# Performance work log

Measured on AMD Instinct MI355X. Metric: run time of the kernel, lower is better.

The kernel has to match this reference:

```python
import jax, jax.numpy as jnp
import numpy as np

B, T, D = 4, 4096, 1024
H = 16
DK = D // H
EPS = 1e-6


def _phi(x):
    return jax.nn.elu(x) + 1.0


def setup_inputs() -> dict:
    key = jax.random.key(0)
    ks = jax.random.split(key, 9)
    s = 1.0 / np.sqrt(D)
    return {
        "x": jax.random.normal(ks[0], (B, T, D), dtype=jnp.float32),
        "Wq": jax.random.uniform(ks[1], (D, D), jnp.float32, -s, s),
        "bq": jax.random.uniform(ks[2], (D,), jnp.float32, -s, s),
        "Wk": jax.random.uniform(ks[3], (D, D), jnp.float32, -s, s),
        "bk": jax.random.uniform(ks[4], (D,), jnp.float32, -s, s),
        "Wv": jax.random.uniform(ks[5], (D, D), jnp.float32, -s, s),
        "bv": jax.random.uniform(ks[6], (D,), jnp.float32, -s, s),
        "Wo": jax.random.uniform(ks[7], (D, D), jnp.float32, -s, s),
        "bo": jax.random.uniform(ks[8], (D,), jnp.float32, -s, s),
    }


def reference(x, Wq, bq, Wk, bk, Wv, bv, Wo, bo):
    Bq, Tq, _ = x.shape

    def heads(y):  # [B,T,D] -> [B,H,T,DK]
        return y.reshape(Bq, Tq, H, DK).transpose(0, 2, 1, 3)

    q = _phi(heads(x @ Wq.T + bq))
    k = _phi(heads(x @ Wk.T + bk))
    v = heads(x @ Wv.T + bv)

    # associative KV summary: [B,H,DK,DK]
    kv = jnp.einsum("bhtd,bhtm->bhdm", k, v)
    # normalizer: q . (sum_t k + eps), then +eps, reciprocal
    z = 1.0 / (jnp.einsum("bhtd,bhd->bht", q, k.sum(axis=2) + EPS) + EPS)
    out = jnp.einsum("bhtd,bhdm,bht->bhtm", q, kv, z)

    out = out.transpose(0, 2, 1, 3).reshape(Bq, Tq, -1)  # [B,T,D]
    return out @ Wo.T + bo
```

## Files before the change

### kernel.cpp

```cpp
#include <hip/hip_runtime.h>
#include <cstdint>
#include <cstddef>

typedef unsigned short u16;
typedef __bf16 bf16x8 __attribute__((ext_vector_type(8)));
typedef float  f32x4  __attribute__((ext_vector_type(4)));
typedef u16    u16x8v __attribute__((ext_vector_type(8)));
typedef u16    u16x4  __attribute__((ext_vector_type(4)));

#define EPS 1e-6f

__device__ __forceinline__ u16 f2bf(float f) {
  union { float f; unsigned int u; } v; v.f = f;
  unsigned int u = v.u + 0x7FFFu + ((v.u >> 16) & 1u);
  return (u16)(u >> 16);
}
__device__ __forceinline__ float bf2f(u16 h) {
  union { unsigned int u; float f; } v; v.u = ((unsigned int)h) << 16;
  return v.f;
}
__device__ __forceinline__ void async16(const void* g, void* l) {
  __builtin_amdgcn_global_load_lds(
      (const __attribute__((address_space(1))) void*)g,
      (__attribute__((address_space(3))) void*)l, 16, 0, 0);
}

__global__ __launch_bounds__(256) void cvt_all_kernel(
    const float* __restrict__ x,
    const float* __restrict__ w0, const float* __restrict__ w1,
    const float* __restrict__ w2, const float* __restrict__ w3,
    u16* __restrict__ xb, u16* __restrict__ o0, u16* __restrict__ o1,
    u16* __restrict__ o2, u16* __restrict__ o3) {
  const int gb = blockIdx.x;
  const float* in;
  u16* out;
  int i;
  if (gb < 8192) {
    in = x; out = xb; i = gb * 256 + threadIdx.x;
  } else {
    const int wb = gb - 8192;
    in  = (wb < 512) ? w0 : (wb < 1024) ? w1 : (wb < 1536) ? w2 : w3;
    out = (wb < 512) ? o0 : (wb < 1024) ? o1 : (wb < 1536) ? o2 : o3;
    i = (wb & 511) * 256 + threadIdx.x;
  }
  const float4* p = (const float4*)in;
  float4 a = p[2 * (size_t)i], b = p[2 * (size_t)i + 1];
  u16x8v o;
  o[0] = f2bf(a.x); o[1] = f2bf(a.y); o[2] = f2bf(a.z); o[3] = f2bf(a.w);
  o[4] = f2bf(b.x); o[5] = f2bf(b.y); o[6] = f2bf(b.z); o[7] = f2bf(b.w);
  *(u16x8v*)(out + 8 * (size_t)i) = o;
}

template <int MODE>
__global__ __launch_bounds__(512) void gemm4r(
    const u16* __restrict__ A, const u16* __restrict__ Bw,
    const float* __restrict__ bias0, const float* __restrict__ bias1,
    const float* __restrict__ bias2,
    u16* __restrict__ O0, u16* __restrict__ O1, u16* __restrict__ O2,
    float* __restrict__ Of, int K) {
  __shared__ u16 sA[2][256 * 64];
  __shared__ u16 sB[2][256 * 64];

  const int tid = threadIdx.x, wave = tid >> 6, lane = tid & 63;
  const int bm = blockIdx.x * 256, bn = blockIdx.y * 256;
  const int wmh = (wave >> 2) * 64;
  const int wq  = (wave & 3) * 32;
  const int l15 = lane & 15, l4 = lane >> 4, l7 = lane & 7;

  f32x4 acc[8][4] = {};

  const int trow = tid >> 3;
  const int sch8 = ((tid & 7) ^ (trow & 7)) * 8;

#define STG_A(buf, qm, s, kt)                                                 \
  async16(A + (size_t)(bm + (s)*128 + (qm)*64 + trow) * K + (kt) + sch8,      \
          &sA[buf][(((qm)*128 + (s)*64) + wave * 8) * 64])
#define STG_B(buf, qn, s, kt)                                                 \
  async16(Bw + (size_t)(bn + ((s)*2 + (trow >> 5)) * 64 + (qn)*32 +           \
                        (trow & 31)) * K + (kt) + sch8,                       \
          &sB[buf][(((qn)*128 + (s)*64) + wave * 8) * 64])

  bf16x8 af[4][2], bq[4][2];

#define RD_A(buf, qm)                                                         \
  _Pragma("unroll") for (int m = 0; m < 4; m++)                               \
    _Pragma("unroll") for (int kk = 0; kk < 2; kk++)                          \
      af[m][kk] = *(const bf16x8*)&sA[buf][((qm)*128 + wmh + m * 16 + l15) * 64 \
                                           + ((kk * 4 + l4) ^ l7) * 8];
#define RD_B(buf)                                                             \
  _Pragma("unroll") for (int nf = 0; nf < 4; nf++)                            \
    _Pragma("unroll") for (int kk = 0; kk < 2; kk++)                          \
      bq[nf][kk] = *(const bf16x8*)&sB[buf][((nf >> 1) * 128 + wq +           \
                                            (nf & 1) * 16 + l15) * 64 +       \
                                           ((kk * 4 + l4) ^ l7) * 8];

#define WAITV_(n) asm volatile("s_waitcnt vmcnt(" #n ")" ::: "memory")
#define WAITV(n) WAITV_(n)

#define PH_EXEC_(qm, W)                                                       \
  _Pragma("unroll") for (int kk = 0; kk < 2; kk++)                            \
    _Pragma("unroll") for (int m = 0; m < 4; m++)                             \
      _Pragma("unroll") for (int nf = 0; nf < 4; nf++)                        \
        acc[(qm)*4 + m][nf] = __builtin_amdgcn_mfma_f32_16x16x32_bf16(        \
            af[m][kk], bq[nf][kk], acc[(qm)*4 + m][nf], 0, 0, 0);             \
  asm volatile("s_waitcnt vmcnt(" #W ") lgkmcnt(0)" ::: "memory");            \
  __builtin_amdgcn_s_barrier();                                               \
  asm volatile("" ::: "memory");
#define PH_EXEC(qm, W) PH_EXEC_(qm, W)

#define ITER_BODY(kO, kE2, kO2, hasT2, hasT3, W0, W1, W2, W3)                 \
                  \
  RD_B(0); RD_A(0, 0);                                                        \
  STG_A(1, 1, 0, kO); STG_A(1, 1, 1, kO);                                     \
  PH_EXEC(0, W0);                                                             \
                                      \
  RD_A(0, 1);                                                                 \
  if (hasT2) {                                                                \
    STG_B(0, 0, 0, kE2); STG_B(0, 0, 1, kE2);                                 \
    STG_B(0, 1, 0, kE2); STG_B(0, 1, 1, kE2);                                 \
    STG_A(0, 0, 0, kE2); STG_A(0, 0, 1, kE2);                                 \
  }                                                                           \
  PH_EXEC(1, W1);                                                             \
                             \
  RD_B(1); RD_A(1, 0);                                                        \
  if (hasT2) { STG_A(0, 1, 0, kE2); STG_A(0, 1, 1, kE2); }                    \
  PH_EXEC(0, W2);                                                             \
                                      \
  RD_A(1, 1);                                                                 \
  if (hasT3) {                                                                \
    STG_B(1, 0, 0, kO2); STG_B(1, 0, 1, kO2);                                 \
    STG_B(1, 1, 0, kO2); STG_B(1, 1, 1, kO2);                                 \
    STG_A(1, 0, 0, kO2); STG_A(1, 0, 1, kO2);                                 \
  }                                                                           \
  PH_EXEC(1, W3);

  STG_B(0, 0, 0, 0);  STG_B(0, 0, 1, 0);  STG_B(0, 1, 0, 0);  STG_B(0, 1, 1, 0);
  STG_A(0, 0, 0, 0);  STG_A(0, 0, 1, 0);
  STG_A(0, 1, 0, 0);  STG_A(0, 1, 1, 0);
  STG_B(1, 0, 0, 64); STG_B(1, 0, 1, 64); STG_B(1, 1, 0, 64); STG_B(1, 1, 1, 64);
  STG_A(1, 0, 0, 64); STG_A(1, 0, 1, 64);
  WAITV(6);
  __builtin_amdgcn_s_barrier();
  asm volatile("" ::: "memory");

  const int NT = K >> 6;
  const int NI = NT >> 1;
  for (int i = 0; i < NI - 1; ++i) {
    const int kO  = (2 * i + 1) * 64;
    const int kE2 = (2 * i + 2) * 64;
    const int kO2 = (2 * i + 3) * 64;
    ITER_BODY(kO, kE2, kO2, true, true, 8, 8, 8, 8);
  }
  {
    const int kO = (NT - 1) * 64;
    ITER_BODY(kO, 0, 0, false, false, 8, 2, 0, 0);
  }
#undef STG_A
#undef STG_B
#undef RD_A
#undef RD_B
#undef WAITV
#undef WAITV_
#undef PH_EXEC
#undef PH_EXEC_
#undef ITER_BODY

  const int wm = wmh * 2;
  const int wn = (wave & 3) * 64;
  const int r0 = l4 * 4, cc = l15;
  if constexpr (MODE == 1) {
    const int mat = blockIdx.y >> 2;
    u16* outp = (mat == 0) ? O0 : (mat == 1) ? O1 : O2;
    const float* bias = (mat == 0) ? bias0 : (mat == 1) ? bias1 : bias2;
    const int act = (mat < 2);
    const int colb = (blockIdx.y & 3) * 256;
    float bvv[4];
#pragma unroll
    for (int ni = 0; ni < 4; ni++) bvv[ni] = bias[colb + wn + ni * 16 + cc];
#pragma unroll
    for (int mi = 0; mi < 8; mi++) {
#pragma unroll
      for (int j = 0; j < 4; j++) {
        const int row = bm + wm + mi * 16 + r0 + j;
#pragma unroll
        for (int ni = 0; ni < 4; ni++) {
          const int col = colb + wn + ni * 16 + cc;
          float val = acc[mi][ni][j] + bvv[ni];
          if (act) val = (val > 0.f) ? (val + 1.f) : __expf(val);
          outp[(size_t)row * 1024 + col] = f2bf(val);
        }
      }
    }
  } else {
    float bvv[4];
#pragma unroll
    for (int ni = 0; ni < 4; ni++) bvv[ni] = bias0[bn + wn + ni * 16 + cc];
#pragma unroll
    for (int mi = 0; mi < 8; mi++) {
#pragma unroll
      for (int j = 0; j < 4; j++) {
        const int row = bm + wm + mi * 16 + r0 + j;
#pragma unroll
        for (int ni = 0; ni < 4; ni++) {
          const int col = bn + wn + ni * 16 + cc;
          Of[(size_t)row * 1024 + col] = acc[mi][ni][j] + bvv[ni];
        }
      }
    }
  }
}

__global__ __launch_bounds__(256) void kv_mfma_kernel(
    const u16* __restrict__ Kb, const u16* __restrict__ Vb,
    float* __restrict__ kv_part, float* __restrict__ ksum_part) {
  const int bh = blockIdx.y;
  const int chunk = blockIdx.x;
  const int b = bh >> 4, h = bh & 15;
  const int tid = threadIdx.x, wave = tid >> 6, lane = tid & 63;

  __shared__ u16 sKT[64 * 64];
  __shared__ u16 sVT[64 * 64];

  f32x4 acc[4] = {};
  f32x4 accs[4] = {};

  union { u16x8v u; bf16x8 b; } uo;
#pragma unroll
  for (int e = 0; e < 8; e++) uo.u[e] = 0x3F80;
  const bf16x8 ones = uo.b;

  const int half = tid >> 7;
  const int j    = tid & 127;
  const int tg   = j >> 3;
  const int dg   = j & 7;
  const u16* src = half ? Vb : Kb;
  u16* dst = half ? sVT : sKT;
  const int colb = (4 * tg + 8 * dg) & 63;

  const size_t rowBase = (size_t)b * 4096 + (size_t)chunk * 512;
  const size_t gbase = (rowBase + 4 * tg) * 1024 + (size_t)h * 64 + dg * 8;

  u16x8v pre[2][4];
#pragma unroll
  for (int s = 0; s < 4; s++)
    pre[0][s] = *(const u16x8v*)(src + gbase + (size_t)s * 1024);

#pragma unroll
  for (int st = 0; st < 8; st++) {
    const int cb = st & 1;
    __syncthreads();
#pragma unroll
    for (int e = 0; e < 8; e++) {
      u16x4 w;
      w[0] = pre[cb][0][e]; w[1] = pre[cb][1][e];
      w[2] = pre[cb][2][e]; w[3] = pre[cb][3][e];
      *(u16x4*)&dst[(dg * 8 + e) * 64 + colb] = w;
    }
    if (st + 1 < 8) {
      const size_t nb = gbase + (size_t)(st + 1) * 64 * 1024;
#pragma unroll
      for (int s = 0; s < 4; s++)
        pre[cb ^ 1][s] = *(const u16x8v*)(src + nb + (size_t)s * 1024);
    }
    __syncthreads();

#pragma unroll
    for (int kst = 0; kst < 2; kst++) {
      const int q8 = kst * 32 + (lane >> 4) * 8;
      bf16x8 bfrag;
      {
        const int rr = wave * 16 + (lane & 15);
        const int c = (q8 + 8 * (rr >> 3)) & 63;
        bfrag = *(const bf16x8*)&sVT[rr * 64 + c];
      }
#pragma unroll
      for (int i = 0; i < 4; i++) {
        const int rr = i * 16 + (lane & 15);
        const int c = (q8 + 8 * (rr >> 3)) & 63;
        const bf16x8 afrag = *(const bf16x8*)&sKT[rr * 64 + c];
        acc[i] = __builtin_amdgcn_mfma_f32_16x16x32_bf16(afrag, bfrag, acc[i], 0, 0, 0);
        if (wave == 0)
          accs[i] = __builtin_amdgcn_mfma_f32_16x16x32_bf16(afrag, ones, accs[i], 0, 0, 0);
      }
    }
  }

  const int r0 = (lane >> 4) * 4, cc = lane & 15;
  float* kvp = kv_part + ((size_t)chunk * 64 + bh) * 4096;
#pragma unroll
  for (int i = 0; i < 4; i++)
#pragma unroll
    for (int jj = 0; jj < 4; jj++)
      kvp[(size_t)(i * 16 + r0 + jj) * 64 + wave * 16 + cc] = acc[i][jj];
  if (wave == 0 && cc == 0) {
#pragma unroll
    for (int i = 0; i < 4; i++)
#pragma unroll
      for (int jj = 0; jj < 4; jj++)
        ksum_part[((size_t)chunk * 64 + bh) * 64 + i * 16 + r0 + jj] = accs[i][jj];
  }
}

__global__ __launch_bounds__(256) void kv_reduce_kernel(
    const float* __restrict__ kv_part, const float* __restrict__ ksum_part,
    u16* __restrict__ kvbf, float* __restrict__ ksum) {
  const int bh = blockIdx.x;
  const int tid = threadIdx.x;
#pragma unroll
  for (int it = 0; it < 4; it++) {
    const int idx = it * 1024 + tid * 4;
    float4 s = {0.f, 0.f, 0.f, 0.f};
#pragma unroll
    for (int c = 0; c < 8; c++) {
      const float4 p = *(const float4*)&kv_part[((size_t)c * 64 + bh) * 4096 + idx];
      s.x += p.x; s.y += p.y; s.z += p.z; s.w += p.w;
    }
    u16x4 o;
    o[0] = f2bf(s.x); o[1] = f2bf(s.y); o[2] = f2bf(s.z); o[3] = f2bf(s.w);
    *(u16x4*)&kvbf[(size_t)bh * 4096 + idx] = o;
  }
  if (tid < 64) {
    float s = 0.f;
#pragma unroll
    for (int c = 0; c < 8; c++)
      s += ksum_part[((size_t)c * 64 + bh) * 64 + tid];
    ksum[(size_t)bh * 64 + tid] = s;
  }
}

#define QST 80
__global__ __launch_bounds__(256) void attn_apply_kernel(
    const u16* __restrict__ Qb, const u16* __restrict__ kvbf,
    const float* __restrict__ ksum, u16* __restrict__ attn) {
  const int bh = blockIdx.y;
  const int t4 = blockIdx.x;
  const int b = bh >> 4, h = bh & 15;
  const int tid = threadIdx.x, wave = tid >> 6, lane = tid & 63;

  __shared__ u16 skvT[64 * QST];
  __shared__ u16 sq[64 * QST];
  __shared__ float sz[64];
  __shared__ float sks[64];
  __shared__ float szp[256];

  if (tid < 64) sks[tid] = ksum[(size_t)bh * 64 + tid] + EPS;
  const u16* kvp = kvbf + (size_t)bh * 4096;
  for (int i = tid; i < 4096; i += 256) {
    const int dd = i >> 6, mm = i & 63;
    skvT[mm * QST + dd] = kvp[i];
  }

  const size_t qbase0 = ((size_t)b * 4096 + (size_t)t4 * 256) * 1024 + h * 64;

  for (int st = 0; st < 4; ++st) {
    const size_t qbase = qbase0 + (size_t)st * 64 * 1024;
    __syncthreads();
    for (int i = tid; i < 4096; i += 256) {
      const int r = i >> 6, dd = i & 63;
      sq[r * QST + dd] = Qb[qbase + (size_t)r * 1024 + dd];
    }
    __syncthreads();

    {
      const int zr = tid & 63, zg = tid >> 6;
      float pz = 0.f;
#pragma unroll
      for (int jj = 0; jj < 16; jj++) {
        const int dd = zg * 16 + jj;
        pz += bf2f(sq[zr * QST + dd]) * sks[dd];
      }
      szp[zg * 64 + zr] = pz;
    }
    __syncthreads();
    if (tid < 64)
      sz[tid] = 1.f / (szp[tid] + szp[64 + tid] + szp[128 + tid] + szp[192 + tid] + EPS);
    __syncthreads();

    f32x4 acc[4] = {};
#pragma unroll
    for (int ks2 = 0; ks2 < 2; ks2++) {
      const bf16x8 a = *(const bf16x8*)&sq[(wave * 16 + (lane & 15)) * QST + ks2 * 32 + (lane >> 4) * 8];
#pragma unroll
      for (int ni = 0; ni < 4; ni++) {
        const bf16x8 bv = *(const bf16x8*)&skvT[(ni * 16 + (lane & 15)) * QST + ks2 * 32 + (lane >> 4) * 8];
        acc[ni] = __builtin_amdgcn_mfma_f32_16x16x32_bf16(a, bv, acc[ni], 0, 0, 0);
      }
    }

    const int r0 = (lane >> 4) * 4, cc = lane & 15;
#pragma unroll
    for (int ni = 0; ni < 4; ni++) {
#pragma unroll
      for (int j = 0; j < 4; j++) {
        const int r = wave * 16 + r0 + j;
        const int c = ni * 16 + cc;
        const float val = acc[ni][j] * sz[r];
        attn[qbase + (size_t)r * 1024 + c] = f2bf(val);
      }
    }
  }
}

extern "C" void kernel_launch(void* const* d_in, const int* in_sizes, int n_in,
                              void* d_out, int out_size, void* d_ws, size_t ws_size,
                              hipStream_t stream) {
  (void)in_sizes; (void)n_in; (void)out_size; (void)ws_size;
  const float* x  = (const float*)d_in[0];
  const float* Wq = (const float*)d_in[1];
  const float* bq = (const float*)d_in[2];
  const float* Wk = (const float*)d_in[3];
  const float* bk = (const float*)d_in[4];
  const float* Wv = (const float*)d_in[5];
  const float* bv = (const float*)d_in[6];
  const float* Wo = (const float*)d_in[7];
  const float* bo = (const float*)d_in[8];

  char* ws = (char*)d_ws;
  u16* xb    = (u16*)ws;  ws += 33554432;
  u16* wqkvb = (u16*)ws;  ws += 6291456;
  u16* wob   = (u16*)ws;  ws += 2097152;
  u16* Vb    = (u16*)ws;  ws += 33554432;
  u16* attn  = (u16*)ws;  ws += 33554432;
  float* kv_part   = (float*)ws; ws += 8388608;
  float* ksum_part = (float*)ws; ws += 131072;
  u16*   kvbf      = (u16*)ws;   ws += 524288;
  float* ksum      = (float*)ws; ws += 16384;

  u16* Qb = (u16*)d_out;
  u16* Kb = Qb + 16777216;

  cvt_all_kernel<<<10240, 256, 0, stream>>>(x, Wq, Wk, Wv, Wo,
                                            xb, wqkvb, wqkvb + 1048576,
                                            wqkvb + 2097152, wob);

  gemm4r<1><<<dim3(64, 12), 512, 0, stream>>>(
      xb, wqkvb, bq, bk, bv, Qb, Kb, Vb, nullptr, 1024);

  kv_mfma_kernel<<<dim3(8, 64), dim3(256), 0, stream>>>(Kb, Vb, kv_part, ksum_part);
  kv_reduce_kernel<<<64, 256, 0, stream>>>(kv_part, ksum_part, kvbf, ksum);
  attn_apply_kernel<<<dim3(16, 64), dim3(256), 0, stream>>>(Qb, kvbf, ksum, attn);

  gemm4r<0><<<dim3(64, 4), 512, 0, stream>>>(
      attn, wob, bo, nullptr, nullptr, nullptr, nullptr, nullptr,
      (float*)d_out, 1024);
}
```

Before: 295.7 us.

## Split KV summary into more chunks, pre-transpose KV, vectorize attn loads

Doubles the number of time chunks in the KV-summary kernel (16 chunks of 256 rows), so more blocks run in parallel, and reduces 16 partials instead of 8. The reduce kernel now writes KV transposed via shared memory, so the apply kernel can load it and Q with 16-byte vector loads instead of scalar loads. The partial buffer reuses the attn workspace, which is safe because attn is written only later. The cost is more partial traffic in the reduce step.

After: 295.1 us. Within noise of the previous version (-0.2%).

```diff
diff --git a/kernel.cpp b/kernel.cpp
--- a/kernel.cpp
+++ b/kernel.cpp
@@ -109,11 +109,9 @@
 #define PH_EXEC(qm, W) PH_EXEC_(qm, W)
 
 #define ITER_BODY(kO, kE2, kO2, hasT2, hasT3, W0, W1, W2, W3)                 \
-                  \
   RD_B(0); RD_A(0, 0);                                                        \
   STG_A(1, 1, 0, kO); STG_A(1, 1, 1, kO);                                     \
   PH_EXEC(0, W0);                                                             \
-                                      \
   RD_A(0, 1);                                                                 \
   if (hasT2) {                                                                \
     STG_B(0, 0, 0, kE2); STG_B(0, 0, 1, kE2);                                 \
@@ -121,11 +119,9 @@
     STG_A(0, 0, 0, kE2); STG_A(0, 0, 1, kE2);                                 \
   }                                                                           \
   PH_EXEC(1, W1);                                                             \
-                             \
   RD_B(1); RD_A(1, 0);                                                        \
   if (hasT2) { STG_A(0, 1, 0, kE2); STG_A(0, 1, 1, kE2); }                    \
   PH_EXEC(0, W2);                                                             \
-                                      \
   RD_A(1, 1);                                                                 \
   if (hasT3) {                                                                \
     STG_B(1, 0, 0, kO2); STG_B(1, 0, 1, kO2);                                 \
@@ -237,7 +233,7 @@
   u16* dst = half ? sVT : sKT;
   const int colb = (4 * tg + 8 * dg) & 63;
 
-  const size_t rowBase = (size_t)b * 4096 + (size_t)chunk * 512;
+  const size_t rowBase = (size_t)b * 4096 + (size_t)chunk * 256;
   const size_t gbase = (rowBase + 4 * tg) * 1024 + (size_t)h * 64 + dg * 8;
 
   u16x8v pre[2][4];
@@ -246,7 +242,7 @@
     pre[0][s] = *(const u16x8v*)(src + gbase + (size_t)s * 1024);
 
 #pragma unroll
-  for (int st = 0; st < 8; st++) {
+  for (int st = 0; st < 4; st++) {
     const int cb = st & 1;
     __syncthreads();
 #pragma unroll
@@ -256,7 +252,7 @@
       w[2] = pre[cb][2][e]; w[3] = pre[cb][3][e];
       *(u16x4*)&dst[(dg * 8 + e) * 64 + colb] = w;
     }
-    if (st + 1 < 8) {
+    if (st + 1 < 4) {
       const size_t nb = gbase + (size_t)(st + 1) * 64 * 1024;
 #pragma unroll
       for (int s = 0; s < 4; s++)
@@ -303,26 +299,39 @@
 
 __global__ __launch_bounds__(256) void kv_reduce_kernel(
     const float* __restrict__ kv_part, const float* __restrict__ ksum_part,
-    u16* __restrict__ kvbf, float* __restrict__ ksum) {
+    u16* __restrict__ kvbfT, float* __restrict__ ksum) {
   const int bh = blockIdx.x;
   const int tid = threadIdx.x;
+  __shared__ float sfull[64][65];
 #pragma unroll
   for (int it = 0; it < 4; it++) {
     const int idx = it * 1024 + tid * 4;
     float4 s = {0.f, 0.f, 0.f, 0.f};
 #pragma unroll
-    for (int c = 0; c < 8; c++) {
+    for (int c = 0; c < 16; c++) {
       const float4 p = *(const float4*)&kv_part[((size_t)c * 64 + bh) * 4096 + idx];
       s.x += p.x; s.y += p.y; s.z += p.z; s.w += p.w;
     }
-    u16x4 o;
-    o[0] = f2bf(s.x); o[1] = f2bf(s.y); o[2] = f2bf(s.z); o[3] = f2bf(s.w);
-    *(u16x4*)&kvbf[(size_t)bh * 4096 + idx] = o;
+    const int d = idx >> 6, m0 = idx & 63;
+    sfull[d][m0] = s.x; sfull[d][m0 + 1] = s.y;
+    sfull[d][m0 + 2] = s.z; sfull[d][m0 + 3] = s.w;
+  }
+  __syncthreads();
+  {
+    const int m = tid >> 2, dq = (tid & 3) * 16;
+    u16x8v o0, o1;
+#pragma unroll
+    for (int e = 0; e < 8; e++) {
+      o0[e] = f2bf(sfull[dq + e][m]);
+      o1[e] = f2bf(sfull[dq + 8 + e][m]);
+    }
+    *(u16x8v*)&kvbfT[(size_t)bh * 4096 + m * 64 + dq]     = o0;
+    *(u16x8v*)&kvbfT[(size_t)bh * 4096 + m * 64 + dq + 8] = o1;
   }
   if (tid < 64) {
     float s = 0.f;
 #pragma unroll
-    for (int c = 0; c < 8; c++)
+    for (int c = 0; c < 16; c++)
       s += ksum_part[((size_t)c * 64 + bh) * 64 + tid];
     ksum[(size_t)bh * 64 + tid] = s;
   }
@@ -330,7 +339,7 @@
 
 #define QST 80
 __global__ __launch_bounds__(256) void attn_apply_kernel(
-    const u16* __restrict__ Qb, const u16* __restrict__ kvbf,
+    const u16* __restrict__ Qb, const u16* __restrict__ kvbfT,
     const float* __restrict__ ksum, u16* __restrict__ attn) {
   const int bh = blockIdx.y;
   const int t4 = blockIdx.x;
@@ -344,10 +353,10 @@
   __shared__ float szp[256];
 
   if (tid < 64) sks[tid] = ksum[(size_t)bh * 64 + tid] + EPS;
-  const u16* kvp = kvbf + (size_t)bh * 4096;
-  for (int i = tid; i < 4096; i += 256) {
-    const int dd = i >> 6, mm = i & 63;
-    skvT[mm * QST + dd] = kvp[i];
+  const u16* kvp = kvbfT + (size_t)bh * 4096;
+  for (int i = tid; i < 512; i += 256) {
+    const int mm = i >> 3, d8 = (i & 7) * 8;
+    *(u16x8v*)&skvT[mm * QST + d8] = *(const u16x8v*)&kvp[mm * 64 + d8];
   }
 
   const size_t qbase0 = ((size_t)b * 4096 + (size_t)t4 * 256) * 1024 + h * 64;
@@ -355,9 +364,10 @@
   for (int st = 0; st < 4; ++st) {
     const size_t qbase = qbase0 + (size_t)st * 64 * 1024;
     __syncthreads();
-    for (int i = tid; i < 4096; i += 256) {
-      const int r = i >> 6, dd = i & 63;
-      sq[r * QST + dd] = Qb[qbase + (size_t)r * 1024 + dd];
+    for (int i = tid; i < 512; i += 256) {
+      const int r = i >> 3, d8 = (i & 7) * 8;
+      *(u16x8v*)&sq[r * QST + d8] =
+          *(const u16x8v*)&Qb[qbase + (size_t)r * 1024 + d8];
     }
     __syncthreads();
 
@@ -421,10 +431,11 @@
   u16* wob   = (u16*)ws;  ws += 2097152;
   u16* Vb    = (u16*)ws;  ws += 33554432;
   u16* attn  = (u16*)ws;  ws += 33554432;
-  float* kv_part   = (float*)ws; ws += 8388608;
-  float* ksum_part = (float*)ws; ws += 131072;
-  u16*   kvbf      = (u16*)ws;   ws += 524288;
+  float* ksum_part = (float*)ws; ws += 262144;
+  u16*   kvbfT     = (u16*)ws;   ws += 524288;
   float* ksum      = (float*)ws; ws += 16384;
+
+  float* kv_part = (float*)attn;
 
   u16* Qb = (u16*)d_out;
   u16* Kb = Qb + 16777216;
@@ -436,9 +447,9 @@
   gemm4r<1><<<dim3(64, 12), 512, 0, stream>>>(
       xb, wqkvb, bq, bk, bv, Qb, Kb, Vb, nullptr, 1024);
 
-  kv_mfma_kernel<<<dim3(8, 64), dim3(256), 0, stream>>>(Kb, Vb, kv_part, ksum_part);
-  kv_reduce_kernel<<<64, 256, 0, stream>>>(kv_part, ksum_part, kvbf, ksum);
-  attn_apply_kernel<<<dim3(16, 64), dim3(256), 0, stream>>>(Qb, kvbf, ksum, attn);
+  kv_mfma_kernel<<<dim3(16, 64), dim3(256), 0, stream>>>(Kb, Vb, kv_part, ksum_part);
+  kv_reduce_kernel<<<64, 256, 0, stream>>>(kv_part, ksum_part, kvbfT, ksum);
+  attn_apply_kernel<<<dim3(16, 64), dim3(256), 0, stream>>>(Qb, kvbfT, ksum, attn);
 
   gemm4r<0><<<dim3(64, 4), 512, 0, stream>>>(
       attn, wob, bo, nullptr, nullptr, nullptr, nullptr, nullptr,
```
